# Performance work log

Hardware: AMD Instinct MI355X
Metric: run time of the kernel (lower is better)

Reference implementation:

```python
import jax, jax.numpy as jnp
import numpy as np

DIM, NH, NKV, HD = 4096, 32, 8, 128
N_REP = NH // NKV
START_POS = 32767  # decode position; cache holds positions [0, START_POS)


def _rope(x, cos, sin):
    # x: (B, L, H, D); cos/sin: (L, D/2). Complex multiply on (even, odd) pairs.
    b, l, h, d = x.shape
    xr = x.reshape(b, l, h, d // 2, 2)
    x0, x1 = xr[..., 0], xr[..., 1]
    c = cos[None, :, None, :]
    s = sin[None, :, None, :]
    o0 = x0 * c - x1 * s
    o1 = x0 * s + x1 * c
    return jnp.stack([o0, o1], axis=-1).reshape(b, l, h, d)


def setup_inputs() -> dict:
    key = jax.random.key(0)
    ks = jax.random.split(key, 8)
    x = jax.random.normal(ks[0], (1, 1, DIM), jnp.float32)
    # real RoPE angles for the current position
    inv_freq = 1.0 / (10000.0 ** (np.arange(0, HD, 2, dtype=np.float32) / HD))
    ang = jnp.asarray((START_POS * inv_freq)[None, :], jnp.float32)  # (1, 64)
    freqs_cos = jnp.cos(ang)
    freqs_sin = jnp.sin(ang)
    k_cache = jax.random.normal(ks[1], (START_POS, NKV, HD), jnp.float32)
    v_cache = jax.random.normal(ks[2], (START_POS, NKV, HD), jnp.float32)
    sd = 1.0 / np.sqrt(DIM)
    wq = jax.random.normal(ks[3], (NH * HD, DIM), jnp.float32) * sd
    wk = jax.random.normal(ks[4], (NKV * HD, DIM), jnp.float32) * sd
    wv = jax.random.normal(ks[5], (NKV * HD, DIM), jnp.float32) * sd
    wo = jax.random.normal(ks[6], (DIM, NH * HD), jnp.float32) * sd
    return {"x": x, "freqs_cos": freqs_cos, "freqs_sin": freqs_sin,
            "k_cache": k_cache, "v_cache": v_cache,
            "wq": wq, "wk": wk, "wv": wv, "wo": wo,
            "start_pos": START_POS}


def reference(x, freqs_cos, freqs_sin, k_cache, v_cache, wq, wk, wv, wo, start_pos):
    bsz, seqlen, _ = x.shape  # (1, 1, DIM)
    q = (x @ wq.T).reshape(bsz, seqlen, NH, HD)
    k = (x @ wk.T).reshape(bsz, seqlen, NKV, HD)
    v = (x @ wv.T).reshape(bsz, seqlen, NKV, HD)
    q = _rope(q, freqs_cos, freqs_sin)
    k = _rope(k, freqs_cos, freqs_sin)
    # push current token KV and fetch full history (offloader fetch over all
    # blocks 0..start_pos//BLOCK == plain concat of cache + current token)
    k_full = jnp.concatenate([k_cache, k[0]], axis=0)  # (T, NKV, HD), T = start_pos+1
    v_full = jnp.concatenate([v_cache, v[0]], axis=0)
    # GQA repeat_kv: (T, NKV, HD) -> (1, NH, T, HD)
    T = k_full.shape[0]
    k_h = jnp.repeat(k_full, N_REP, axis=1).transpose(1, 0, 2)[None]  # (1, NH, T, HD)
    v_h = jnp.repeat(v_full, N_REP, axis=1).transpose(1, 0, 2)[None]
    qh = q.transpose(0, 2, 1, 3)  # (1, NH, 1, HD)
    scores = jnp.einsum("bhqd,bhtd->bhqt", qh, k_h) / jnp.sqrt(jnp.float32(HD))
    probs = jax.nn.softmax(scores, axis=-1)
    out = jnp.einsum("bhqt,bhtd->bhqd", probs, v_h)  # (1, NH, 1, HD)
    out = out.transpose(0, 2, 1, 3).reshape(bsz, seqlen, NH * HD)
    return out @ wo.T
```

## Files before the change

### kernel.cpp

```cpp
#include <hip/hip_runtime.h>
#include <math.h>

#define DIM 4096
#define NH 32
#define NKV 8
#define HD 128
#define NREP 4
#define RSPLIT 128

typedef float f32x4 __attribute__((ext_vector_type(4)));

__global__ __launch_bounds__(256) void qkv_rope_kernel(
    const float* __restrict__ x, const float* __restrict__ fc,
    const float* __restrict__ fs, const float* __restrict__ wq,
    const float* __restrict__ wk, const float* __restrict__ wv,
    float* __restrict__ q_rope, float* __restrict__ k_new,
    float* __restrict__ v_new, float* __restrict__ attn_raw) {
  if (blockIdx.x == 0) {
    for (int i = threadIdx.x; i < NH * HD + NH; i += 256) attn_raw[i] = 0.f;
  }
  int wave = blockIdx.x * 4 + (threadIdx.x >> 6);
  int lane = threadIdx.x & 63;
  const float* W;
  float* dst;
  int r0;
  bool rope;
  if (wave < 2048) {
    W = wq; dst = q_rope; r0 = wave * 2; rope = true;
  } else if (wave < 2560) {
    W = wk; dst = k_new; r0 = (wave - 2048) * 2; rope = true;
  } else {
    W = wv; dst = v_new; r0 = (wave - 2560) * 2; rope = false;
  }
  const float4* x4 = (const float4*)x;
  const float4* w0 = (const float4*)(W + (size_t)r0 * DIM);
  const float4* w1 = (const float4*)(W + (size_t)(r0 + 1) * DIM);
  float a0 = 0.f, a1 = 0.f;
#pragma unroll 4
  for (int c = lane; c < DIM / 4; c += 64) {
    float4 xv = x4[c];
    float4 u = w0[c];
    float4 v = w1[c];
    a0 += xv.x * u.x + xv.y * u.y + xv.z * u.z + xv.w * u.w;
    a1 += xv.x * v.x + xv.y * v.y + xv.z * v.z + xv.w * v.w;
  }
  for (int off = 32; off > 0; off >>= 1) {
    a0 += __shfl_down(a0, off, 64);
    a1 += __shfl_down(a1, off, 64);
  }
  if (lane == 0) {
    if (rope) {
      int j = (r0 & (HD - 1)) >> 1;
      float c = fc[j], s = fs[j];
      dst[r0]     = a0 * c - a1 * s;
      dst[r0 + 1] = a0 * s + a1 * c;
    } else {
      dst[r0]     = a0;
      dst[r0 + 1] = a1;
    }
  }
}

#define LD4(p) (*(const float4*)(p))
#define NT4(p) (__builtin_nontemporal_load((const f32x4*)(p)))

#define DOT4(sv, h)                                                         \
  sv = A.x * qf[h][0] + A.y * qf[h][1] + A.z * qf[h][2] + A.w * qf[h][3] +  \
       B.x * qf[h][4] + B.y * qf[h][5] + B.z * qf[h][6] + B.w * qf[h][7];

#define PV8(h, e)                                                           \
  acc[h][0] += (e)*VA.x; acc[h][1] += (e)*VA.y;                             \
  acc[h][2] += (e)*VA.z; acc[h][3] += (e)*VA.w;                             \
  acc[h][4] += (e)*VB.x; acc[h][5] += (e)*VB.y;                             \
  acc[h][6] += (e)*VB.z; acc[h][7] += (e)*VB.w;

#define STEP(KA_, KB_, VA_, VB_, VALID)                                     \
  {                                                                         \
    auto A = KA_; auto B = KB_;                                             \
    float s0, s1, s2, s3;                                                   \
    DOT4(s0, 0); DOT4(s1, 1); DOT4(s2, 2); DOT4(s3, 3);                     \
    float pp = hi8 ? s2 : s0, pq = hi8 ? s0 : s2;                           \
    pp += __shfl_xor(pq, 8, 64);                                            \
    float rr = hi8 ? s3 : s1, rs = hi8 ? s1 : s3;                           \
    rr += __shfl_xor(rs, 8, 64);                                            \
    float u = hi4 ? rr : pp, uvx = hi4 ? pp : rr;                           \
    u += __shfl_xor(uvx, 4, 64);                                            \
    u += __shfl_xor(u, 1, 64);                                              \
    u += __shfl_xor(u, 2, 64);                                              \
    float u4 = __shfl_xor(u, 4, 64);                                        \
    float u8 = __shfl_xor(u, 8, 64);                                        \
    float u12 = __shfl_xor(u4, 8, 64);                                      \
    float q0 = hi4 ? u4 : u,   q1 = hi4 ? u : u4;                           \
    float q2 = hi4 ? u12 : u8, q3 = hi4 ? u8 : u12;                         \
    float w0 = hi8 ? q2 : q0, w1 = hi8 ? q3 : q1;                           \
    float w2 = hi8 ? q0 : q2, w3 = hi8 ? q1 : q3;                           \
    float e0 = __expf((VALID) ? w0 * scale : -1e30f);                       \
    float e1 = __expf((VALID) ? w1 * scale : -1e30f);                       \
    float e2 = __expf((VALID) ? w2 * scale : -1e30f);                       \
    float e3 = __expf((VALID) ? w3 * scale : -1e30f);                       \
    lsum[0] += e0; lsum[1] += e1; lsum[2] += e2; lsum[3] += e3;             \
    auto VA = VA_; auto VB = VB_;                                           \
    PV8(0, e0) PV8(1, e1) PV8(2, e2) PV8(3, e3)                             \
  }

__global__ __launch_bounds__(256, 4) void attn_partial_kernel(
    const float* __restrict__ q_rope, const float* __restrict__ k_cache,
    const float* __restrict__ v_cache, const float* __restrict__ k_new,
    const float* __restrict__ v_new, float* __restrict__ attn_raw,
    float* __restrict__ L_raw, int start_pos, int T, int CH) {
  int g = blockIdx.x % NKV;
  int split = blockIdx.x / NKV;
  int t0 = split * CH;
  int tid = threadIdx.x;
  int wvi = tid >> 6;
  int lane = tid & 63;
  int grp = lane >> 4;
  int lig = lane & 15;
  int tl0 = wvi * 4 + grp;
  int dbase = lig * 8;
  bool hi8 = (lig & 8) != 0, hi4 = (lig & 4) != 0;

  __shared__ float s_wacc[4][4][HD];
  __shared__ float s_wl[4][4];

  float qf[4][8];
#pragma unroll
  for (int h = 0; h < 4; ++h)
#pragma unroll
    for (int e = 0; e < 8; ++e)
      qf[h][e] = q_rope[(g * NREP + h) * HD + dbase + e];

  float lsum[4] = {0.f, 0.f, 0.f, 0.f};
  float acc[4][8];
#pragma unroll
  for (int h = 0; h < 4; ++h)
#pragma unroll
    for (int e = 0; e < 8; ++e) acc[h][e] = 0.f;

  const float scale = 0.08838834764831845f;
  int iters = CH >> 4;
  bool full = (t0 + CH + 16 <= start_pos);
  const size_t kstep = (size_t)16 * NKV * HD;

  if (full) {
    const float* kp = k_cache + ((size_t)(t0 + tl0) * NKV + g) * HD + dbase;
    const float* vp = v_cache + ((size_t)(t0 + tl0) * NKV + g) * HD + dbase;
    f32x4 KA0 = NT4(kp), KB0 = NT4(kp + 4);
    f32x4 VA0 = NT4(vp), VB0 = NT4(vp + 4);
    kp += kstep; vp += kstep;
    for (int i = 0; i < iters; i += 2) {
      f32x4 KA1 = NT4(kp), KB1 = NT4(kp + 4);
      f32x4 VA1 = NT4(vp), VB1 = NT4(vp + 4);
      kp += kstep; vp += kstep;
      __builtin_amdgcn_sched_barrier(0);
      STEP(KA0, KB0, VA0, VB0, true);
      KA0 = NT4(kp); KB0 = NT4(kp + 4);
      VA0 = NT4(vp); VB0 = NT4(vp + 4);
      kp += kstep; vp += kstep;
      __builtin_amdgcn_sched_barrier(0);
      STEP(KA1, KB1, VA1, VB1, true);
    }
  } else {
    for (int i = 0; i < iters; ++i) {
      int t = t0 + i * 16 + tl0;
      bool valid = (t < T);
      const float* kp;
      const float* vp;
      if (t < start_pos) {
        kp = k_cache + ((size_t)t * NKV + g) * HD;
        vp = v_cache + ((size_t)t * NKV + g) * HD;
      } else {
        kp = k_new + (size_t)g * HD;
        vp = v_new + (size_t)g * HD;
      }
      f32x4 KA = NT4(kp + dbase), KB = NT4(kp + dbase + 4);
      f32x4 VAx = NT4(vp + dbase), VBx = NT4(vp + dbase + 4);
      STEP(KA, KB, VAx, VBx, valid);
    }
  }

#pragma unroll
  for (int h = 0; h < 4; ++h) {
    float lh = lsum[h];
    lh += __shfl_xor(lh, 16, 64);
    lh += __shfl_xor(lh, 32, 64);
    lsum[h] = lh;
#pragma unroll
    for (int e = 0; e < 8; ++e) {
      float a = acc[h][e];
      a += __shfl_xor(a, 16, 64);
      a += __shfl_xor(a, 32, 64);
      acc[h][e] = a;
    }
  }
  if (grp == 0) {
#pragma unroll
    for (int h = 0; h < 4; ++h)
#pragma unroll
      for (int e = 0; e < 8; ++e) s_wacc[wvi][h][dbase + e] = acc[h][e];
    if (lig == 0) {
#pragma unroll
      for (int h = 0; h < 4; ++h) s_wl[wvi][h] = lsum[h];
    }
  }
  __syncthreads();
  for (int o = tid; o < NREP * HD; o += 256) {
    int h = o >> 7, d = o & (HD - 1);
    float sum = s_wacc[0][h][d] + s_wacc[1][h][d] + s_wacc[2][h][d] +
                s_wacc[3][h][d];
    atomicAdd(&attn_raw[(g * NREP + h) * HD + d], sum);
  }
  if (tid < NREP) {
    atomicAdd(&L_raw[g * NREP + tid],
              s_wl[0][tid] + s_wl[1][tid] + s_wl[2][tid] + s_wl[3][tid]);
  }
}

__global__ __launch_bounds__(256) void out_gemv_kernel(
    const float* __restrict__ attn_raw, const float* __restrict__ L_raw,
    const float* __restrict__ wo, float* __restrict__ out) {
  __shared__ float s_invL[NH];
  if (threadIdx.x < NH) s_invL[threadIdx.x] = 1.f / L_raw[threadIdx.x];
  __syncthreads();
  int row = blockIdx.x * 4 + (threadIdx.x >> 6);
  int lane = threadIdx.x & 63;
  const float4* a4 = (const float4*)attn_raw;
  const float4* w4 = (const float4*)(wo + (size_t)row * DIM);
  float a = 0.f;
#pragma unroll 4
  for (int c = lane; c < DIM / 4; c += 64) {
    float4 av = a4[c];
    float4 wv = w4[c];
    float il = s_invL[c >> 5];
    a += (av.x * wv.x + av.y * wv.y + av.z * wv.z + av.w * wv.w) * il;
  }
  for (int off = 32; off > 0; off >>= 1) a += __shfl_down(a, off, 64);
  if (lane == 0) out[row] = a;
}

extern "C" void kernel_launch(void* const* d_in, const int* in_sizes, int n_in,
                              void* d_out, int out_size, void* d_ws,
                              size_t ws_size, hipStream_t stream) {
  const float* x       = (const float*)d_in[0];
  const float* fc      = (const float*)d_in[1];
  const float* fs      = (const float*)d_in[2];
  const float* k_cache = (const float*)d_in[3];
  const float* v_cache = (const float*)d_in[4];
  const float* wq      = (const float*)d_in[5];
  const float* wk      = (const float*)d_in[6];
  const float* wv      = (const float*)d_in[7];
  const float* wo      = (const float*)d_in[8];
  float* out = (float*)d_out;

  int start_pos = in_sizes[3] / (NKV * HD);
  int T = start_pos + 1;
  int CH = ((T + RSPLIT - 1) / RSPLIT + 15) & ~15;

  float* ws = (float*)d_ws;
  float* q_rope   = ws;
  float* k_new    = ws + 4096;
  float* v_new    = ws + 5120;
  float* attn_raw = ws + 6144;
  float* L_raw    = attn_raw + NH * HD;

  qkv_rope_kernel<<<768, 256, 0, stream>>>(x, fc, fs, wq, wk, wv, q_rope,
                                           k_new, v_new, attn_raw);
  attn_partial_kernel<<<NKV * RSPLIT, 256, 0, stream>>>(
      q_rope, k_cache, v_cache, k_new, v_new, attn_raw, L_raw,
      start_pos, T, CH);
  out_gemv_kernel<<<1024, 256, 0, stream>>>(attn_raw, L_raw, wo, out);
}
```

Baseline: 92.29 us.

## Process two KV groups per attention block with finer time splits

Each attention block now covers two adjacent KV heads instead of one, so each 16-lane group reads 512 contiguous bytes spanning two heads of the same token row. The time axis is split into 256 chunks of 8-token steps, and the block count stays 1024. The aim is more contiguous memory access per wave over the KV cache and fewer cross-lane shuffle reductions. In exchange, each block does twice as many atomic adds, and the per-thread q registers come from two different groups.

```diff
diff --git a/kernel.cpp b/kernel.cpp
--- a/kernel.cpp
+++ b/kernel.cpp
@@ -6,7 +6,7 @@
 #define NKV 8
 #define HD 128
 #define NREP 4
-#define RSPLIT 128
+#define NSPLIT 256
 
 typedef float f32x4 __attribute__((ext_vector_type(4)));
 
@@ -108,20 +108,22 @@
     const float* __restrict__ v_cache, const float* __restrict__ k_new,
     const float* __restrict__ v_new, float* __restrict__ attn_raw,
     float* __restrict__ L_raw, int start_pos, int T, int CH) {
-  int g = blockIdx.x % NKV;
-  int split = blockIdx.x / NKV;
+  int g0 = (blockIdx.x & 3) * 2;
+  int split = blockIdx.x >> 2;
   int t0 = split * CH;
   int tid = threadIdx.x;
   int wvi = tid >> 6;
   int lane = tid & 63;
   int grp = lane >> 4;
   int lig = lane & 15;
-  int tl0 = wvi * 4 + grp;
+  int gsel = grp & 1;
+  int g = g0 + gsel;
+  int tl0 = wvi * 2 + (grp >> 1);
   int dbase = lig * 8;
   bool hi8 = (lig & 8) != 0, hi4 = (lig & 4) != 0;
 
-  __shared__ float s_wacc[4][4][HD];
-  __shared__ float s_wl[4][4];
+  __shared__ float s_wacc[4][2][NREP][HD];
+  __shared__ float s_wl[4][2][NREP];
 
   float qf[4][8];
 #pragma unroll
@@ -138,9 +140,9 @@
     for (int e = 0; e < 8; ++e) acc[h][e] = 0.f;
 
   const float scale = 0.08838834764831845f;
-  int iters = CH >> 4;
-  bool full = (t0 + CH + 16 <= start_pos);
-  const size_t kstep = (size_t)16 * NKV * HD;
+  int iters = CH >> 3;
+  bool full = (t0 + CH + 8 <= start_pos);
+  const size_t kstep = (size_t)8 * NKV * HD;
 
   if (full) {
     const float* kp = k_cache + ((size_t)(t0 + tl0) * NKV + g) * HD + dbase;
@@ -162,7 +164,7 @@
     }
   } else {
     for (int i = 0; i < iters; ++i) {
-      int t = t0 + i * 16 + tl0;
+      int t = t0 + i * 8 + tl0;
       bool valid = (t < T);
       const float* kp;
       const float* vp;
@@ -181,38 +183,33 @@
 
 #pragma unroll
   for (int h = 0; h < 4; ++h) {
-    float lh = lsum[h];
-    lh += __shfl_xor(lh, 16, 64);
-    lh += __shfl_xor(lh, 32, 64);
-    lsum[h] = lh;
-#pragma unroll
-    for (int e = 0; e < 8; ++e) {
-      float a = acc[h][e];
-      a += __shfl_xor(a, 16, 64);
-      a += __shfl_xor(a, 32, 64);
-      acc[h][e] = a;
-    }
-  }
-  if (grp == 0) {
+    lsum[h] += __shfl_xor(lsum[h], 32, 64);
+#pragma unroll
+    for (int e = 0; e < 8; ++e) acc[h][e] += __shfl_xor(acc[h][e], 32, 64);
+  }
+  if (grp < 2) {
 #pragma unroll
     for (int h = 0; h < 4; ++h)
 #pragma unroll
-      for (int e = 0; e < 8; ++e) s_wacc[wvi][h][dbase + e] = acc[h][e];
+      for (int e = 0; e < 8; ++e)
+        s_wacc[wvi][gsel][h][dbase + e] = acc[h][e];
     if (lig == 0) {
 #pragma unroll
-      for (int h = 0; h < 4; ++h) s_wl[wvi][h] = lsum[h];
+      for (int h = 0; h < 4; ++h) s_wl[wvi][gsel][h] = lsum[h];
     }
   }
   __syncthreads();
-  for (int o = tid; o < NREP * HD; o += 256) {
-    int h = o >> 7, d = o & (HD - 1);
-    float sum = s_wacc[0][h][d] + s_wacc[1][h][d] + s_wacc[2][h][d] +
-                s_wacc[3][h][d];
-    atomicAdd(&attn_raw[(g * NREP + h) * HD + d], sum);
-  }
-  if (tid < NREP) {
-    atomicAdd(&L_raw[g * NREP + tid],
-              s_wl[0][tid] + s_wl[1][tid] + s_wl[2][tid] + s_wl[3][tid]);
+  for (int o = tid; o < 2 * NREP * HD; o += 256) {
+    int gs = o >> 9, h = (o >> 7) & 3, d = o & (HD - 1);
+    float sum = s_wacc[0][gs][h][d] + s_wacc[1][gs][h][d] +
+                s_wacc[2][gs][h][d] + s_wacc[3][gs][h][d];
+    atomicAdd(&attn_raw[((g0 + gs) * NREP + h) * HD + d], sum);
+  }
+  if (tid < 2 * NREP) {
+    int gs = tid >> 2, h = tid & 3;
+    atomicAdd(&L_raw[(g0 + gs) * NREP + h],
+              s_wl[0][gs][h] + s_wl[1][gs][h] + s_wl[2][gs][h] +
+                  s_wl[3][gs][h]);
   }
 }
 
@@ -254,7 +251,7 @@
 
   int start_pos = in_sizes[3] / (NKV * HD);
   int T = start_pos + 1;
-  int CH = ((T + RSPLIT - 1) / RSPLIT + 15) & ~15;
+  int CH = ((T + NSPLIT - 1) / NSPLIT + 7) & ~7;
 
   float* ws = (float*)d_ws;
   float* q_rope   = ws;
@@ -265,7 +262,7 @@
 
   qkv_rope_kernel<<<768, 256, 0, stream>>>(x, fc, fs, wq, wk, wv, q_rope,
                                            k_new, v_new, attn_raw);
-  attn_partial_kernel<<<NKV * RSPLIT, 256, 0, stream>>>(
+  attn_partial_kernel<<<4 * NSPLIT, 256, 0, stream>>>(
       q_rope, k_cache, v_cache, k_new, v_new, attn_raw, L_raw,
       start_pos, T, CH);
   out_gemv_kernel<<<1024, 256, 0, stream>>>(attn_raw, L_raw, wo, out);
```

After: 88.88 us (median of 2 runs). 3.7% less time.
